# Performance work log

Hardware: AMD Instinct MI355X
Metric: run time of the kernel (lower is better)

## Reference

```python
import jax, jax.numpy as jnp
import numpy as np
from jax import lax

N = 4096        # num graph nodes
T = 8           # timesteps (LSTM batch dim in original, batch_first=False)
IN_DIM = 64
H = 128         # hidden_dim
OUT_DIM = 1
E_RAND = 65536  # random edges; self-loops appended -> E = 69632


def setup_inputs() -> dict:
    key = jax.random.key(0)
    ks = jax.random.split(key, 18)
    s = 0.05
    f = lambda k, shp: (jax.random.normal(k, shp, jnp.float32) * s)
    src = jnp.concatenate([jax.random.randint(ks[15], (E_RAND,), 0, N), jnp.arange(N)]).astype(jnp.int32)
    dst = jnp.concatenate([jax.random.randint(ks[16], (E_RAND,), 0, N), jnp.arange(N)]).astype(jnp.int32)
    return {
        "input": jax.random.normal(ks[0], (N, T, IN_DIM), jnp.float32),
        "hidden": f(ks[1], (1, T, H)),
        "cell": f(ks[2], (1, T, H)),
        "pre_w": f(ks[3], (IN_DIM, H)),
        "pre_b": f(ks[4], (H,)),
        "w_ih": f(ks[5], (4 * H, H)),
        "w_hh": f(ks[6], (4 * H, H)),
        "b_ih": f(ks[7], (4 * H,)),
        "b_hh": f(ks[8], (4 * H,)),
        "gat_wsrc": f(ks[9], (H, H)),
        "gat_wdst": f(ks[10], (H, H)),
        "gat_attn": f(ks[11], (H,)),
        "gat_b": f(ks[12], (H,)),
        "out_w": f(ks[13], (H, OUT_DIM)),
        "out_b": f(ks[14], (OUT_DIM,)),
        "edge_src": src,
        "edge_dst": dst,
    }


def reference(input, hidden, cell, pre_w, pre_b, w_ih, w_hh, b_ih, b_hh,
              gat_wsrc, gat_wdst, gat_attn, gat_b, out_w, out_b,
              edge_src, edge_dst):
    n_nodes = input.shape[0]
    x = input @ pre_w + pre_b                         # (N, T, H)
    b = b_ih + b_hh

    # LSTM over node dimension (seq = nodes); the T per-timestep runs of the
    # original Python loop are independent (init states come from the given
    # hidden/cell), so we batch them along T.
    def step(carry, x_n):                             # x_n: (T, H)
        h, c = carry
        g = x_n @ w_ih.T + h @ w_hh.T + b             # (T, 4H), torch gate order i,f,g,o
        i_g, f_g, g_g, o_g = jnp.split(g, 4, axis=-1)
        c = jax.nn.sigmoid(f_g) * c + jax.nn.sigmoid(i_g) * jnp.tanh(g_g)
        h = jax.nn.sigmoid(o_g) * jnp.tanh(c)
        return (h, c), h

    (hT, cT), outs = lax.scan(step, (hidden[0], cell[0]), x)   # outs: (N, T, H)

    # GATv2Conv (DGL semantics, num_heads=1, share_weights=False)
    fs = outs @ gat_wsrc                              # (N, T, H)
    fd = outs @ gat_wdst
    e = jax.nn.leaky_relu(fs[edge_src] + fd[edge_dst], 0.2)    # (E, T, H)
    logits = e @ gat_attn                             # (E, T)
    # edge softmax per destination node (numerically stable)
    m = lax.stop_gradient(jax.ops.segment_max(logits, edge_dst, num_segments=n_nodes))
    a = jnp.exp(logits - m[edge_dst])
    denom = jax.ops.segment_sum(a, edge_dst, num_segments=n_nodes)
    alpha = a / denom[edge_dst]                       # (E, T)
    agg = jax.ops.segment_sum(alpha[..., None] * fs[edge_src], edge_dst, num_segments=n_nodes)
    rst = agg + gat_b                                 # (N, T, H)

    # dropout is identity in eval mode
    y = rst @ out_w + out_b                           # (N, T, OUT_DIM)
    return (y, hT[None], cT[None])
```

## Files before the change

### kernel.cpp

```cpp
#include <hip/hip_runtime.h>
#include <hip/hip_bf16.h>

#define N_NODES 4096
#define T_STEPS 8
#define INDIM   64
#define HDIM    128
#define G4      512
#define NROWS   (N_NODES * T_STEPS)
#define LOG2E   1.4426950408889634f

typedef __hip_bfloat16 bf16;
typedef __attribute__((ext_vector_type(8))) short bf16x8;
typedef __attribute__((ext_vector_type(4))) float f32x4;
typedef __attribute__((ext_vector_type(8))) int   i32x8;

__device__ __forceinline__ float asfloat_u(unsigned int u) {
    union { unsigned int i; float f; } v; v.i = u; return v.f;
}
__device__ __forceinline__ float fexp2(float x) {
    float r; asm("v_exp_f32 %0, %1" : "=v"(r) : "v"(x)); return r;
}

#define P_O0 32768
#define P_O1 (P_O0 + 512)
#define P_O2 (P_O1 + 16384)
#define P_O3 (P_O2 + 16384)
#define P_O4 (P_O3 + 128)
#define P_O5 (P_O4 + 1)
#define P_O6 (P_O5 + 65536)
__global__ void prep_kernel(const float* __restrict__ pre_w, const float* __restrict__ pre_b,
                            const float* __restrict__ w_ih, const float* __restrict__ b_ih,
                            const float* __restrict__ b_hh, const float* __restrict__ w_hh,
                            const float* __restrict__ wsrc, const float* __restrict__ wdst,
                            const float* __restrict__ out_w, const float* __restrict__ out_b,
                            const float* __restrict__ gat_b,
                            float* __restrict__ Wc, float* __restrict__ bc,
                            float* __restrict__ wsT, float* __restrict__ wdT,
                            float* __restrict__ wso, float* __restrict__ cy,
                            unsigned char* __restrict__ whh8) {
    int id = blockIdx.x * 256 + threadIdx.x;
    if (id < P_O0) {
        int g = id >> 6, i = id & 63;
        float s = 0.f;
        for (int k = 0; k < HDIM; k++) s += pre_w[i * HDIM + k] * w_ih[g * HDIM + k];
        int gate = g >> 7;
        Wc[id] = s * ((gate == 2) ? -2.f * LOG2E : -LOG2E);
    } else if (id < P_O1) {
        int g = id - P_O0;
        float s = b_ih[g] + b_hh[g];
        for (int k = 0; k < HDIM; k++) s += pre_b[k] * w_ih[g * HDIM + k];
        int gate = g >> 7;
        bc[g] = s * ((gate == 2) ? -2.f * LOG2E : -LOG2E);
    } else if (id < P_O2) {
        int c = id - P_O1;
        int co = c >> 7, k = c & 127;
        wsT[c] = wsrc[k * HDIM + co];
    } else if (id < P_O3) {
        int c = id - P_O2;
        int co = c >> 7, k = c & 127;
        wdT[c] = wdst[k * HDIM + co];
    } else if (id < P_O4) {
        int hi = id - P_O3;
        float s = 0.f;
        for (int ho = 0; ho < HDIM; ho++) s += wsrc[hi * HDIM + ho] * out_w[ho];
        wso[hi] = s;
    } else if (id == P_O4) {
        float s = out_b[0];
        for (int h = 0; h < HDIM; h++) s += gat_b[h] * out_w[h];
        cy[0] = s;
    } else if (id < P_O6) {
        int c = id - P_O5;
        int gate = c >> 14;
        float v = w_hh[c] * ((gate == 2) ? -2.f * LOG2E : -LOG2E);
        int pk = __builtin_amdgcn_cvt_pk_fp8_f32(v, v, 0, false);
        whh8[c] = (unsigned char)(pk & 0xff);
    }
}

__global__ __launch_bounds__(512) void xw_kernel(const float* __restrict__ input,
                                                 const float* __restrict__ Wc,
                                                 const float* __restrict__ bc,
                                                 bf16* __restrict__ xw) {
    __shared__ __align__(16) float in_lds[16 * INDIM];
    int tid = threadIdx.x;
    int rowbase = blockIdx.x * 16;
    in_lds[tid]       = input[(size_t)rowbase * INDIM + tid];
    in_lds[tid + 512] = input[(size_t)rowbase * INDIM + tid + 512];
    __syncthreads();
    int g = tid;
    int gate = g >> 7, hh = g & 127;
    float4 w[16];
    const float4* wr = reinterpret_cast<const float4*>(Wc + g * INDIM);
#pragma unroll
    for (int u = 0; u < 16; u++) w[u] = wr[u];
    float b = bc[g];
    for (int r = 0; r < 16; r++) {
        const float4* hv = reinterpret_cast<const float4*>(in_lds + r * INDIM);
        float a0 = b, a1 = 0.f, a2 = 0.f, a3 = 0.f;
#pragma unroll
        for (int u = 0; u < 16; u++) {
            float4 h4 = hv[u]; float4 wv = w[u];
            a0 = fmaf(h4.x, wv.x, a0); a1 = fmaf(h4.y, wv.y, a1);
            a2 = fmaf(h4.z, wv.z, a2); a3 = fmaf(h4.w, wv.w, a3);
        }
        xw[(size_t)(rowbase + r) * G4 + hh * 4 + gate] = __float2bfloat16((a0 + a1) + (a2 + a3));
    }
}

__global__ __launch_bounds__(512, 1) void lstm_kernel(const bf16* __restrict__ xw,
                                                      const unsigned char* __restrict__ whh8,
                                                      const float* __restrict__ hidden0,
                                                      const float* __restrict__ cell0,
                                                      float* __restrict__ outs,
                                                      float* __restrict__ dout) {
    __shared__ __align__(16) char hbuf0[4 * 144];
    __shared__ __align__(16) char hbuf1[4 * 144];
    const int tid  = threadIdx.x;
    const int w    = tid >> 6;
    const int lane = tid & 63;
    const int kg   = lane >> 4;
    const int lr   = lane & 15;
    const int q    = lr & 3;
    const int d    = lr >> 2;
    const int qg   = blockIdx.x * 4 + q;
    const int hb   = 16 * w + kg * 4 + d;

    i32x8 afr[4];
#pragma unroll
    for (int G = 0; G < 4; G++) {
        const unsigned char* rowp = whh8 + (size_t)(G * 128 + 16 * w + lr) * HDIM + kg * 32;
        afr[G] = *reinterpret_cast<const i32x8*>(rowp);
    }

    const int roff = q * 144 + kg * 32;
    const int woff = q * 144 + hb;
    const int sc   = 0x7f7f7f7f;

    float cv = cell0[qg * HDIM + hb];
    float hv = hidden0[qg * HDIM + hb];
    {
        int pk = __builtin_amdgcn_cvt_pk_fp8_f32(hv, hv, 0, false);
        *reinterpret_cast<unsigned char*>(hbuf0 + woff) = (unsigned char)(pk & 0xff);
    }

    const uint2* xq = reinterpret_cast<const uint2*>(xw) + qg * 128 + hb;
    float* outp = outs + qg * HDIM + hb;

    uint2 xb[8];
#pragma unroll
    for (int i = 0; i < 8; i++) xb[i] = xq[i * 1024];
    __syncthreads();

#define STEPX(NIDX, RB, WB, XQ)                                                      \
    do {                                                                             \
        i32x8 bfr = *reinterpret_cast<const i32x8*>(RB + roff);                      \
        f32x4 z = {0.f, 0.f, 0.f, 0.f};                                              \
        f32x4 acc0 = __builtin_amdgcn_mfma_scale_f32_16x16x128_f8f6f4(               \
            afr[0], bfr, z, 0, 0, 0, sc, 0, sc);                                     \
        f32x4 acc1 = __builtin_amdgcn_mfma_scale_f32_16x16x128_f8f6f4(               \
            afr[1], bfr, z, 0, 0, 0, sc, 0, sc);                                     \
        f32x4 acc2 = __builtin_amdgcn_mfma_scale_f32_16x16x128_f8f6f4(               \
            afr[2], bfr, z, 0, 0, 0, sc, 0, sc);                                     \
        f32x4 acc3 = __builtin_amdgcn_mfma_scale_f32_16x16x128_f8f6f4(               \
            afr[3], bfr, z, 0, 0, 0, sc, 0, sc);                                     \
        float s0 = (d & 2) ? ((d & 1) ? acc0[3] : acc0[2])                           \
                           : ((d & 1) ? acc0[1] : acc0[0]);                          \
        float s1 = (d & 2) ? ((d & 1) ? acc1[3] : acc1[2])                           \
                           : ((d & 1) ? acc1[1] : acc1[0]);                          \
        float s2 = (d & 2) ? ((d & 1) ? acc2[3] : acc2[2])                           \
                           : ((d & 1) ? acc2[1] : acc2[0]);                          \
        float s3 = (d & 2) ? ((d & 1) ? acc3[3] : acc3[2])                           \
                           : ((d & 1) ? acc3[1] : acc3[0]);                          \
        float gi = s0 + asfloat_u((XQ).x << 16);                                     \
        float gf = s1 + asfloat_u((XQ).x & 0xffff0000u);                             \
        float gg = s2 + asfloat_u((XQ).y << 16);                                     \
        float go = s3 + asfloat_u((XQ).y & 0xffff0000u);                             \
        float A = fexp2(gi), C = fexp2(gf), B = fexp2(gg);                           \
        float p = 1.f + A, r = 1.f + B, s = 1.f + C;                                 \
        float pr = p * r;                                                            \
        float num = fmaf(cv, pr, (2.f - r) * s);                                     \
        cv = num * __builtin_amdgcn_rcpf(pr * s);                                    \
        float O = fexp2(go), F = fexp2(cv * (-2.f * LOG2E));                         \
        float po = 1.f + O, rf = 1.f + F;                                            \
        hv = (2.f - rf) * __builtin_amdgcn_rcpf(po * rf);                            \
        int pk = __builtin_amdgcn_cvt_pk_fp8_f32(hv, hv, 0, false);                  \
        *reinterpret_cast<unsigned char*>(WB + woff) = (unsigned char)(pk & 0xff);   \
        outp[(NIDX) * 1024] = hv;                                                    \
        asm volatile("s_waitcnt lgkmcnt(0)" ::: "memory");                           \
        __builtin_amdgcn_s_barrier();                                                \
        __builtin_amdgcn_sched_barrier(0);                                           \
    } while (0)

    for (int n = 0; n < N_NODES; n += 8) {
#pragma unroll
        for (int i = 0; i < 8; i++) {
            if (i & 1) STEPX(n + i, hbuf1, hbuf0, xb[i]);
            else       STEPX(n + i, hbuf0, hbuf1, xb[i]);
            xb[i] = xq[(n + i + 8) * 1024];
        }
    }
#undef STEPX

    dout[NROWS + qg * HDIM + hb] = hv;
    dout[NROWS + T_STEPS * HDIM + qg * HDIM + hb] = cv;
}

__global__ __launch_bounds__(256) void fsfd_kernel(const float* __restrict__ outs,
                                                   const float* __restrict__ wsT,
                                                   const float* __restrict__ wdT,
                                                   bf16* __restrict__ fs,
                                                   bf16* __restrict__ fd) {
    __shared__ __align__(16) float rows[32 * HDIM];
    int tid = threadIdx.x;
    size_t base = (size_t)blockIdx.x * 32 * HDIM;
#pragma unroll
    for (int j = 0; j < 16; j++) rows[tid + j * 256] = outs[base + tid + j * 256];
    __syncthreads();
    int c = tid;
    const float4* wT = reinterpret_cast<const float4*>(
        (c < HDIM) ? (wsT + c * HDIM) : (wdT + (c - HDIM) * HDIM));
    float4 w[32];
#pragma unroll
    for (int u = 0; u < 32; u++) w[u] = wT[u];
    bf16* dst = (c < HDIM) ? (fs + base + c) : (fd + base + (c - HDIM));
    for (int r = 0; r < 32; r++) {
        const float4* hv = reinterpret_cast<const float4*>(rows + r * HDIM);
        float a0 = 0.f, a1 = 0.f, a2 = 0.f, a3 = 0.f;
#pragma unroll
        for (int u = 0; u < 32; u++) {
            float4 h4 = hv[u]; float4 wv = w[u];
            a0 = fmaf(h4.x, wv.x, a0); a1 = fmaf(h4.y, wv.y, a1);
            a2 = fmaf(h4.z, wv.z, a2); a3 = fmaf(h4.w, wv.w, a3);
        }
        dst[(size_t)r * HDIM] = __float2bfloat16((a0 + a1) + (a2 + a3));
    }
}

__global__ __launch_bounds__(256) void fso_kernel(const float* __restrict__ outs,
                                                  const float* __restrict__ wso,
                                                  float* __restrict__ fso) {
    int tid = threadIdx.x;
    int l = tid & 63;
    int row = blockIdx.x * 4 + (tid >> 6);
    float v = outs[(size_t)row * HDIM + l] * wso[l]
            + outs[(size_t)row * HDIM + 64 + l] * wso[64 + l];
#pragma unroll
    for (int m = 32; m >= 1; m >>= 1) v += __shfl_xor(v, m, 64);
    if (l == 0) fso[row] = v;
}

__global__ __launch_bounds__(256) void edge_kernel(const int* __restrict__ esrc,
                                                   const int* __restrict__ edst,
                                                   const bf16* __restrict__ fs,
                                                   const bf16* __restrict__ fd,
                                                   const float* __restrict__ attn,
                                                   const float* __restrict__ fso,
                                                   float* __restrict__ denom,
                                                   float* __restrict__ ynum, int nE) {
    int tid = threadIdx.x;
    int l = tid & 63;
    int e = blockIdx.x * 4 + (tid >> 6);
    if (e >= nE) return;
    int s = esrc[e], d = edst[e];
    float at1 = attn[l], at2 = attn[64 + l];
    const bf16* fsr = fs + (size_t)s * (T_STEPS * HDIM);
    const bf16* fdr = fd + (size_t)d * (T_STEPS * HDIM);
#pragma unroll
    for (int t = 0; t < T_STEPS; t++) {
        float x1 = __bfloat162float(fsr[t * HDIM + l]) + __bfloat162float(fdr[t * HDIM + l]);
        float x2 = __bfloat162float(fsr[t * HDIM + 64 + l]) + __bfloat162float(fdr[t * HDIM + 64 + l]);
        x1 = fmaxf(x1, 0.f) + 0.2f * fminf(x1, 0.f);
        x2 = fmaxf(x2, 0.f) + 0.2f * fminf(x2, 0.f);
        float v = x1 * at1 + x2 * at2;
#pragma unroll
        for (int m = 32; m >= 1; m >>= 1) v += __shfl_xor(v, m, 64);
        if (l == 0) {
            float a = __expf(v);
            atomicAdd(&denom[d * T_STEPS + t], a);
            atomicAdd(&ynum[d * T_STEPS + t], a * fso[s * T_STEPS + t]);
        }
    }
}

__global__ void final_kernel(const float* __restrict__ ynum, const float* __restrict__ denom,
                             const float* __restrict__ cy, float* __restrict__ dout) {
    int i = blockIdx.x * 256 + threadIdx.x;
    if (i < NROWS) dout[i] = ynum[i] / denom[i] + cy[0];
}

extern "C" void kernel_launch(void* const* d_in, const int* in_sizes, int n_in,
                              void* d_out, int out_size, void* d_ws, size_t ws_size,
                              hipStream_t stream) {
    const float* input  = (const float*)d_in[0];
    const float* hidden = (const float*)d_in[1];
    const float* cell   = (const float*)d_in[2];
    const float* pre_w  = (const float*)d_in[3];
    const float* pre_b  = (const float*)d_in[4];
    const float* w_ih   = (const float*)d_in[5];
    const float* w_hh   = (const float*)d_in[6];
    const float* b_ih   = (const float*)d_in[7];
    const float* b_hh   = (const float*)d_in[8];
    const float* wsrc   = (const float*)d_in[9];
    const float* wdst   = (const float*)d_in[10];
    const float* attn   = (const float*)d_in[11];
    const float* gatb   = (const float*)d_in[12];
    const float* outw   = (const float*)d_in[13];
    const float* outb   = (const float*)d_in[14];
    const int*   esrc   = (const int*)d_in[15];
    const int*   edst   = (const int*)d_in[16];
    int nE = in_sizes[15];
    float* dout = (float*)d_out;
    char* ws = (char*)d_ws;

    const size_t o_xw    = 0;
    const size_t o_outs  = 33554432;
    const size_t o_fs    = 50331648;
    const size_t o_fd    = 58720256;
    const size_t o_fso   = 67108864;
    const size_t o_denom = 67239936;
    const size_t o_ynum  = 67371008;
    const size_t o_wc    = 67502080;
    const size_t o_bc    = 67633152;
    const size_t o_wsT   = 67635200;
    const size_t o_wdT   = 67700736;
    const size_t o_wso   = 67766272;
    const size_t o_cy    = 67766784;
    const size_t o_whh8  = o_fs;

    bf16*  xw    = (bf16*)(ws + o_xw);
    float* outs  = (float*)(ws + o_outs);
    bf16*  fs    = (bf16*)(ws + o_fs);
    bf16*  fd    = (bf16*)(ws + o_fd);
    float* fso   = (float*)(ws + o_fso);
    float* denom = (float*)(ws + o_denom);
    float* ynum  = (float*)(ws + o_ynum);
    float* Wc    = (float*)(ws + o_wc);
    float* bc    = (float*)(ws + o_bc);
    float* wsT   = (float*)(ws + o_wsT);
    float* wdT   = (float*)(ws + o_wdT);
    float* wso   = (float*)(ws + o_wso);
    float* cy    = (float*)(ws + o_cy);
    unsigned char* whh8 = (unsigned char*)(ws + o_whh8);

    prep_kernel<<<515, 256, 0, stream>>>(pre_w, pre_b, w_ih, b_ih, b_hh, w_hh, wsrc, wdst,
                                         outw, outb, gatb, Wc, bc, wsT, wdT, wso, cy, whh8);
    xw_kernel<<<2048, 512, 0, stream>>>(input, Wc, bc, xw);
    lstm_kernel<<<2, 512, 0, stream>>>(xw, whh8, hidden, cell, outs, dout);
    fsfd_kernel<<<1024, 256, 0, stream>>>(outs, wsT, wdT, fs, fd);
    fso_kernel<<<8192, 256, 0, stream>>>(outs, wso, fso);
    hipMemsetAsync(ws + o_denom, 0, 262144, stream);
    edge_kernel<<<(nE + 3) / 4, 256, 0, stream>>>(esrc, edst, fs, fd, attn, fso,
                                                  denom, ynum, nE);
    final_kernel<<<128, 256, 0, stream>>>(ynum, denom, cy, dout);
}
```

Measured before the change: 1.693 ms.

## Replace atomic edge scatter with CSR gather per destination node

Builds a CSR layout of edges grouped by destination node using a histogram, scan and scatter pass. The edge kernel becomes one wavefront per destination that accumulates the softmax numerator and denominator in registers, then writes the output directly. This removes the float atomics, the denominator/numerator memset and the separate final kernel. It also folds the fso projection into fsfd_kernel and prescales attn by log2(e) so it can use a hardware exp2. The cost is three extra small launches for the CSR build, and load imbalance across destinations with many incoming edges.

```diff
diff --git a/kernel.cpp b/kernel.cpp
--- a/kernel.cpp
+++ b/kernel.cpp
@@ -28,16 +28,17 @@
 #define P_O4 (P_O3 + 128)
 #define P_O5 (P_O4 + 1)
 #define P_O6 (P_O5 + 65536)
+#define P_O7 (P_O6 + 128)
 __global__ void prep_kernel(const float* __restrict__ pre_w, const float* __restrict__ pre_b,
                             const float* __restrict__ w_ih, const float* __restrict__ b_ih,
                             const float* __restrict__ b_hh, const float* __restrict__ w_hh,
                             const float* __restrict__ wsrc, const float* __restrict__ wdst,
                             const float* __restrict__ out_w, const float* __restrict__ out_b,
-                            const float* __restrict__ gat_b,
+                            const float* __restrict__ gat_b, const float* __restrict__ attn,
                             float* __restrict__ Wc, float* __restrict__ bc,
                             float* __restrict__ wsT, float* __restrict__ wdT,
                             float* __restrict__ wso, float* __restrict__ cy,
-                            unsigned char* __restrict__ whh8) {
+                            unsigned char* __restrict__ whh8, float* __restrict__ attn2) {
     int id = blockIdx.x * 256 + threadIdx.x;
     if (id < P_O0) {
         int g = id >> 6, i = id & 63;
@@ -74,6 +75,9 @@
         float v = w_hh[c] * ((gate == 2) ? -2.f * LOG2E : -LOG2E);
         int pk = __builtin_amdgcn_cvt_pk_fp8_f32(v, v, 0, false);
         whh8[c] = (unsigned char)(pk & 0xff);
+    } else if (id < P_O7) {
+        int c = id - P_O6;
+        attn2[c] = attn[c] * LOG2E;
     }
 }
 
@@ -104,6 +108,43 @@
             a2 = fmaf(h4.z, wv.z, a2); a3 = fmaf(h4.w, wv.w, a3);
         }
         xw[(size_t)(rowbase + r) * G4 + hh * 4 + gate] = __float2bfloat16((a0 + a1) + (a2 + a3));
+    }
+}
+
+__global__ void hist_kernel(const int* __restrict__ edst, int nE, int* __restrict__ cnt) {
+    int i = blockIdx.x * 256 + threadIdx.x;
+    if (i < nE) atomicAdd(&cnt[edst[i]], 1);
+}
+
+__global__ __launch_bounds__(512) void scan_kernel(const int* __restrict__ cnt,
+                                                   int* __restrict__ rowptr) {
+    __shared__ int part[512];
+    int t = threadIdx.x, base = t * 8;
+    int loc[8]; int s = 0;
+#pragma unroll
+    for (int j = 0; j < 8; j++) { loc[j] = s; s += cnt[base + j]; }
+    part[t] = s;
+    __syncthreads();
+    for (int off = 1; off < 512; off <<= 1) {
+        int v = (t >= off) ? part[t - off] : 0;
+        __syncthreads();
+        part[t] += v;
+        __syncthreads();
+    }
+    int pre = part[t] - s;
+#pragma unroll
+    for (int j = 0; j < 8; j++) rowptr[base + j] = pre + loc[j];
+    if (t == 511) rowptr[4096] = part[511];
+}
+
+__global__ void scatter_kernel(const int* __restrict__ esrc, const int* __restrict__ edst,
+                               int nE, const int* __restrict__ rowptr,
+                               int* __restrict__ cnt2, int* __restrict__ ssrc) {
+    int i = blockIdx.x * 256 + threadIdx.x;
+    if (i < nE) {
+        int d = edst[i];
+        int pos = rowptr[d] + atomicAdd(&cnt2[d], 1);
+        ssrc[pos] = esrc[i];
     }
 }
 
@@ -208,8 +249,10 @@
 __global__ __launch_bounds__(256) void fsfd_kernel(const float* __restrict__ outs,
                                                    const float* __restrict__ wsT,
                                                    const float* __restrict__ wdT,
+                                                   const float* __restrict__ wso,
                                                    bf16* __restrict__ fs,
-                                                   bf16* __restrict__ fd) {
+                                                   bf16* __restrict__ fd,
+                                                   float* __restrict__ fso) {
     __shared__ __align__(16) float rows[32 * HDIM];
     int tid = threadIdx.x;
     size_t base = (size_t)blockIdx.x * 32 * HDIM;
@@ -234,58 +277,71 @@
         }
         dst[(size_t)r * HDIM] = __float2bfloat16((a0 + a1) + (a2 + a3));
     }
-}
-
-__global__ __launch_bounds__(256) void fso_kernel(const float* __restrict__ outs,
-                                                  const float* __restrict__ wso,
-                                                  float* __restrict__ fso) {
-    int tid = threadIdx.x;
-    int l = tid & 63;
-    int row = blockIdx.x * 4 + (tid >> 6);
-    float v = outs[(size_t)row * HDIM + l] * wso[l]
-            + outs[(size_t)row * HDIM + 64 + l] * wso[64 + l];
-#pragma unroll
-    for (int m = 32; m >= 1; m >>= 1) v += __shfl_xor(v, m, 64);
-    if (l == 0) fso[row] = v;
-}
-
-__global__ __launch_bounds__(256) void edge_kernel(const int* __restrict__ esrc,
-                                                   const int* __restrict__ edst,
-                                                   const bf16* __restrict__ fs,
-                                                   const bf16* __restrict__ fd,
-                                                   const float* __restrict__ attn,
-                                                   const float* __restrict__ fso,
-                                                   float* __restrict__ denom,
-                                                   float* __restrict__ ynum, int nE) {
-    int tid = threadIdx.x;
-    int l = tid & 63;
-    int e = blockIdx.x * 4 + (tid >> 6);
-    if (e >= nE) return;
-    int s = esrc[e], d = edst[e];
-    float at1 = attn[l], at2 = attn[64 + l];
-    const bf16* fsr = fs + (size_t)s * (T_STEPS * HDIM);
-    const bf16* fdr = fd + (size_t)d * (T_STEPS * HDIM);
-#pragma unroll
-    for (int t = 0; t < T_STEPS; t++) {
-        float x1 = __bfloat162float(fsr[t * HDIM + l]) + __bfloat162float(fdr[t * HDIM + l]);
-        float x2 = __bfloat162float(fsr[t * HDIM + 64 + l]) + __bfloat162float(fdr[t * HDIM + 64 + l]);
-        x1 = fmaxf(x1, 0.f) + 0.2f * fminf(x1, 0.f);
-        x2 = fmaxf(x2, 0.f) + 0.2f * fminf(x2, 0.f);
-        float v = x1 * at1 + x2 * at2;
-#pragma unroll
-        for (int m = 32; m >= 1; m >>= 1) v += __shfl_xor(v, m, 64);
-        if (l == 0) {
-            float a = __expf(v);
-            atomicAdd(&denom[d * T_STEPS + t], a);
-            atomicAdd(&ynum[d * T_STEPS + t], a * fso[s * T_STEPS + t]);
+    if (tid < 32) {
+        const float* rp = rows + tid * HDIM;
+        float s = 0.f;
+        for (int k = 0; k < HDIM; k++) {
+            int kk = (k + tid) & 127;
+            s += rp[kk] * wso[kk];
         }
-    }
-}
-
-__global__ void final_kernel(const float* __restrict__ ynum, const float* __restrict__ denom,
-                             const float* __restrict__ cy, float* __restrict__ dout) {
-    int i = blockIdx.x * 256 + threadIdx.x;
-    if (i < NROWS) dout[i] = ynum[i] / denom[i] + cy[0];
+        fso[blockIdx.x * 32 + tid] = s;
+    }
+}
+
+__global__ __launch_bounds__(64) void edge_csr_kernel(const int* __restrict__ ssrc,
+                                                      const int* __restrict__ rowptr,
+                                                      const bf16* __restrict__ fs,
+                                                      const bf16* __restrict__ fd,
+                                                      const float* __restrict__ attn2,
+                                                      const float* __restrict__ fso,
+                                                      const float* __restrict__ cy,
+                                                      float* __restrict__ dout) {
+    int dn = blockIdx.x;
+    int l  = threadIdx.x;
+    float a0 = attn2[2 * l], a1 = attn2[2 * l + 1];
+    const unsigned int* fdp = reinterpret_cast<const unsigned int*>(fd) + (size_t)dn * 512 + l;
+    unsigned int fdw[8];
+#pragma unroll
+    for (int t = 0; t < 8; t++) fdw[t] = fdp[t * 64];
+    float den[8], num[8];
+#pragma unroll
+    for (int t = 0; t < 8; t++) { den[t] = 0.f; num[t] = 0.f; }
+    int e0 = rowptr[dn], e1 = rowptr[dn + 1];
+    for (int e = e0; e < e1; e++) {
+        int s = ssrc[e];
+        const unsigned int* fsp = reinterpret_cast<const unsigned int*>(fs) + (size_t)s * 512 + l;
+        float4 fsoA = *reinterpret_cast<const float4*>(fso + s * 8);
+        float4 fsoB = *reinterpret_cast<const float4*>(fso + s * 8 + 4);
+        float fsov[8] = {fsoA.x, fsoA.y, fsoA.z, fsoA.w, fsoB.x, fsoB.y, fsoB.z, fsoB.w};
+#pragma unroll
+        for (int t = 0; t < 8; t++) {
+            unsigned int uf = fsp[t * 64];
+            float x1 = asfloat_u(uf << 16) + asfloat_u(fdw[t] << 16);
+            float x2 = asfloat_u(uf & 0xffff0000u) + asfloat_u(fdw[t] & 0xffff0000u);
+            x1 = fmaxf(x1, 0.f) + 0.2f * fminf(x1, 0.f);
+            x2 = fmaxf(x2, 0.f) + 0.2f * fminf(x2, 0.f);
+            float v = x1 * a0 + x2 * a1;
+#pragma unroll
+            for (int m = 32; m >= 1; m >>= 1) v += __shfl_xor(v, m, 64);
+            float a = fexp2(v);
+            den[t] += a;
+            num[t] = fmaf(a, fsov[t], num[t]);
+        }
+    }
+    if (l == 0) {
+        float cyv = cy[0];
+        float4 y0, y1;
+        y0.x = num[0] * __builtin_amdgcn_rcpf(den[0]) + cyv;
+        y0.y = num[1] * __builtin_amdgcn_rcpf(den[1]) + cyv;
+        y0.z = num[2] * __builtin_amdgcn_rcpf(den[2]) + cyv;
+        y0.w = num[3] * __builtin_amdgcn_rcpf(den[3]) + cyv;
+        y1.x = num[4] * __builtin_amdgcn_rcpf(den[4]) + cyv;
+        y1.y = num[5] * __builtin_amdgcn_rcpf(den[5]) + cyv;
+        y1.z = num[6] * __builtin_amdgcn_rcpf(den[6]) + cyv;
+        y1.w = num[7] * __builtin_amdgcn_rcpf(den[7]) + cyv;
+        *reinterpret_cast<float4*>(dout + dn * 8)     = y0;
+        *reinterpret_cast<float4*>(dout + dn * 8 + 4) = y1;
+    }
 }
 
 extern "C" void kernel_launch(void* const* d_in, const int* in_sizes, int n_in,
@@ -317,14 +373,17 @@
     const size_t o_fs    = 50331648;
     const size_t o_fd    = 58720256;
     const size_t o_fso   = 67108864;
-    const size_t o_denom = 67239936;
-    const size_t o_ynum  = 67371008;
+    const size_t o_cnt   = 67239936;
+    const size_t o_cnt2  = 67256320;
+    const size_t o_rowptr= 67272704;
+    const size_t o_ssrc  = 67289344;
     const size_t o_wc    = 67502080;
     const size_t o_bc    = 67633152;
     const size_t o_wsT   = 67635200;
     const size_t o_wdT   = 67700736;
     const size_t o_wso   = 67766272;
     const size_t o_cy    = 67766784;
+    const size_t o_attn2 = 67767040;
     const size_t o_whh8  = o_fs;
 
     bf16*  xw    = (bf16*)(ws + o_xw);
@@ -332,24 +391,28 @@
     bf16*  fs    = (bf16*)(ws + o_fs);
     bf16*  fd    = (bf16*)(ws + o_fd);
     float* fso   = (float*)(ws + o_fso);
-    float* denom = (float*)(ws + o_denom);
-    float* ynum  = (float*)(ws + o_ynum);
+    int*   cnt   = (int*)(ws + o_cnt);
+    int*   cnt2  = (int*)(ws + o_cnt2);
+    int*   rowptr= (int*)(ws + o_rowptr);
+    int*   ssrc  = (int*)(ws + o_ssrc);
     float* Wc    = (float*)(ws + o_wc);
     float* bc    = (float*)(ws + o_bc);
     float* wsT   = (float*)(ws + o_wsT);
     float* wdT   = (float*)(ws + o_wdT);
     float* wso   = (float*)(ws + o_wso);
     float* cy    = (float*)(ws + o_cy);
+    float* attn2 = (float*)(ws + o_attn2);
     unsigned char* whh8 = (unsigned char*)(ws + o_whh8);
 
-    prep_kernel<<<515, 256, 0, stream>>>(pre_w, pre_b, w_ih, b_ih, b_hh, w_hh, wsrc, wdst,
-                                         outw, outb, gatb, Wc, bc, wsT, wdT, wso, cy, whh8);
+    prep_kernel<<<516, 256, 0, stream>>>(pre_w, pre_b, w_ih, b_ih, b_hh, w_hh, wsrc, wdst,
+                                         outw, outb, gatb, attn,
+                                         Wc, bc, wsT, wdT, wso, cy, whh8, attn2);
     xw_kernel<<<2048, 512, 0, stream>>>(input, Wc, bc, xw);
+    hipMemsetAsync(ws + o_cnt, 0, 32768, stream);
+    hist_kernel<<<(nE + 255) / 256, 256, 0, stream>>>(edst, nE, cnt);
+    scan_kernel<<<1, 512, 0, stream>>>(cnt, rowptr);
+    scatter_kernel<<<(nE + 255) / 256, 256, 0, stream>>>(esrc, edst, nE, rowptr, cnt2, ssrc);
     lstm_kernel<<<2, 512, 0, stream>>>(xw, whh8, hidden, cell, outs, dout);
-    fsfd_kernel<<<1024, 256, 0, stream>>>(outs, wsT, wdT, fs, fd);
-    fso_kernel<<<8192, 256, 0, stream>>>(outs, wso, fso);
-    hipMemsetAsync(ws + o_denom, 0, 262144, stream);
-    edge_kernel<<<(nE + 3) / 4, 256, 0, stream>>>(esrc, edst, fs, fd, attn, fso,
-                                                  denom, ynum, nE);
-    final_kernel<<<128, 256, 0, stream>>>(ynum, denom, cy, dout);
-}
+    fsfd_kernel<<<1024, 256, 0, stream>>>(outs, wsT, wdT, wso, fs, fd, fso);
+    edge_csr_kernel<<<N_NODES, 64, 0, stream>>>(ssrc, rowptr, fs, fd, attn2, fso, cy, dout);
+}
```

Result: no change. 1.685 ms (-0.4%).
